# Kernel tuning notes

Hardware: AMD Instinct MI355X
Metric: run time of the kernel (lower is better)

The kernel has to match this reference:

```python
import jax, jax.numpy as jnp
import numpy as np

NEG = -1000000000.0
EPS = 1e-05

def setup_inputs() -> dict:
    key = jax.random.key(0)
    k1, k2, k3, k4, k5 = jax.random.split(key, 5)
    B, L, E, Q = 64, 2048, 512, 256
    encoded_vecs = jax.random.normal(k1, (B, L, E), dtype=jnp.float32)
    query = jax.random.normal(k2, (B, Q), dtype=jnp.float32)
    length = jax.random.randint(k3, (B,), 1, L + 1, dtype=jnp.int32)
    # Xavier-normal-ish params
    W1 = jax.random.normal(k4, (E + Q, E), dtype=jnp.float32) * jnp.sqrt(2.0 / (E + Q + E))
    b1 = jnp.zeros((E,), dtype=jnp.float32)
    v = jax.random.normal(k5, (E,), dtype=jnp.float32) * jnp.sqrt(2.0 / (E + 1))
    return {"encoded_vecs": encoded_vecs, "query": query, "length": length,
            "W1": W1, "b1": b1, "v": v}

def reference(encoded_vecs, query, length, W1, b1, v):
    B, L, E = encoded_vecs.shape
    # broadcast 2D query over the length dim (repeat in torch code)
    q = jnp.broadcast_to(query[:, None, :], (B, L, query.shape[-1]))
    h = jnp.concatenate([encoded_vecs, q], axis=2)            # [B, L, E+Q]
    u = jnp.tanh(jnp.einsum('blc,ce->ble', h, W1) + b1)       # [B, L, E]
    logits = jnp.einsum('ble,e->bl', u, v)                    # [B, L]
    # masked softmax (faithful to masked_softmax in source)
    mask = (jnp.arange(L)[None, :] < length[:, None])         # [B, L] bool
    masked_logits = jnp.where(mask, logits, NEG)
    max_logits = jnp.max(masked_logits, axis=1, keepdims=True)
    exps = jnp.exp(masked_logits - max_logits) * mask.astype(logits.dtype)
    attention = exps / (jnp.sum(exps, axis=1, keepdims=True) + EPS)  # [B, L]
    context = jnp.einsum('bl,ble->be', attention, encoded_vecs)      # [B, E]
    return (context, attention)
```

## Files before the change

### kernel.cpp

```cpp
#include <hip/hip_runtime.h>

typedef __attribute__((ext_vector_type(4))) float float4v;
typedef __attribute__((ext_vector_type(2))) float float2v;
typedef __attribute__((ext_vector_type(8))) short short8;
typedef __attribute__((ext_vector_type(4))) float f32x4;

#define NEGV (-1000000000.0f)

#define MTOT (64 * 2048)

__device__ __forceinline__ unsigned short f2bf(float f) {
    unsigned int u = __float_as_uint(f);
    u += 0x7fffu + ((u >> 16) & 1u);
    return (unsigned short)(u >> 16);
}

__device__ __forceinline__ void gload_lds16(const void* g, void* l) {
    __builtin_amdgcn_global_load_lds(
        (__attribute__((address_space(1))) unsigned int*)(unsigned long long)(g),
        (__attribute__((address_space(3))) unsigned int*)(unsigned int)(unsigned long long)(l),
        16, 0, 0);
}

__global__ __launch_bounds__(256)
void prep_wt_kernel(const float* __restrict__ W1, unsigned short* __restrict__ Wt) {
    __shared__ float t[32][33];
    int bx = blockIdx.x & 15;
    int by = blockIdx.x >> 4;
    int tx = threadIdx.x & 31;
    int ty = threadIdx.x >> 5;
    #pragma unroll
    for (int i = 0; i < 4; ++i)
        t[ty + 8 * i][tx] = W1[(bx * 32 + ty + 8 * i) * 512 + by * 32 + tx];
    __syncthreads();
    #pragma unroll
    for (int i = 0; i < 4; ++i)
        Wt[(by * 32 + ty + 8 * i) * 512 + bx * 32 + tx] = f2bf(t[tx][ty + 8 * i]);
}

__global__ void prep_qc_kernel(const float* __restrict__ query, const float* __restrict__ W1,
                               const float* __restrict__ b1, float* __restrict__ qc,
                               float* __restrict__ ctxraw, float* __restrict__ S) {
    int b = blockIdx.x;
    int e = threadIdx.x;
    ctxraw[b * 512 + e] = 0.f;
    ctxraw[b * 512 + 256 + e] = 0.f;
    if (e == 0) S[b] = 0.f;
    float acc0 = b1[e];
    float acc1 = b1[e + 256];
    const float* w = W1 + 512 * 512;
    #pragma unroll 8
    for (int q = 0; q < 256; ++q) {
        float qv = query[b * 256 + q];
        acc0 += qv * w[q * 512 + e];
        acc1 += qv * w[q * 512 + e + 256];
    }
    qc[b * 512 + e] = acc0;
    qc[b * 512 + e + 256] = acc1;
}

__global__ __launch_bounds__(1024)
void gemm_fused_kernel(const float* __restrict__ A,
                       const unsigned short* __restrict__ Wt,
                       const float* __restrict__ qc,
                       const float* __restrict__ v,
                       const int* __restrict__ length,
                       float* __restrict__ att,
                       float* __restrict__ ctxraw,
                       float* __restrict__ S)
{
    int bm = blockIdx.x;
    int b = bm >> 4;
    int len = length[b];
    int l0 = (bm & 15) * 128;
    if (l0 >= len) return;

    __shared__ char smem[73728];
    unsigned short* As = (unsigned short*)smem;
    unsigned short* Bs = (unsigned short*)(smem + 8192);
    float (*lred)[8] = (float(*)[8])(smem + 8192);
    float* wbuf = (float*)(smem + 8192 + 4096);

    int tid = threadIdx.x;
    int lane = tid & 63;
    int w = tid >> 6;
    int wm = w >> 3, wn = w & 7;
    long row0 = (long)bm * 128;

    int ar_r = tid >> 3;
    int ar_e = tid & 7;
    const char* gAr = (const char*)A + (row0 + ar_r) * 2048 + ar_e * 16;
    int awr = ar_r * 64 + ((ar_e * 8) ^ (((ar_r >> 1) & 3) << 4));

    int offw = w * 2048 + lane * 16;
    const char* gB0;
    const char* gB1;
    {
        int o = offw;
        int r = o >> 6;
        gB0 = (const char*)Wt + r * 1024 + ((o & 63) ^ (((r >> 1) & 3) << 4));
        o = offw + 1024;
        r = o >> 6;
        gB1 = (const char*)Wt + r * 1024 + ((o & 63) ^ (((r >> 1) & 3) << 4));
    }

    int aoff[4], boff[4];
    int kb = 16 * (lane >> 4);
    #pragma unroll
    for (int mi = 0; mi < 4; ++mi) {
        int ar = wm * 64 + (lane & 15) + mi * 16;
        aoff[mi] = ar * 64 + (kb ^ (((ar >> 1) & 3) << 4));
    }
    #pragma unroll
    for (int ni = 0; ni < 4; ++ni) {
        int br = wn * 64 + (lane & 15) + ni * 16;
        boff[ni] = br * 64 + (kb ^ (((br >> 1) & 3) << 4));
    }

    f32x4 acc[4][4] = {};
    float4v P;

#define GISSUE(t, sI) do {                                                   \
    P = *(const float4v*)(gAr + (t) * 128);                                  \
    char* lb_ = (char*)Bs + (sI) * 32768 + offw;                             \
    gload_lds16(gB0 + (t) * 64, lb_);                                        \
    gload_lds16(gB1 + (t) * 64, lb_ + 1024);                                 \
} while (0)

#define CVTW() do {                                                          \
    union { unsigned int u[2]; unsigned long long ll; } pk_;                 \
    pk_.u[0] = (unsigned int)f2bf(P[0]) | ((unsigned int)f2bf(P[1]) << 16);  \
    pk_.u[1] = (unsigned int)f2bf(P[2]) | ((unsigned int)f2bf(P[3]) << 16);  \
    *(unsigned long long*)((char*)As + awr) = pk_.ll;                        \
} while (0)

#define KCOMP(sC) do {                                                       \
    const char* as_ = (const char*)As;                                       \
    const char* bs_ = (const char*)Bs + (sC) * 32768;                        \
    short8 af_[4];                                                           \
    _Pragma("unroll")                                                        \
    for (int mi = 0; mi < 4; ++mi) af_[mi] = *(const short8*)(as_ + aoff[mi]); \
    _Pragma("unroll")                                                        \
    for (int ni = 0; ni < 4; ++ni) {                                         \
        short8 bf_ = *(const short8*)(bs_ + boff[ni]);                       \
        _Pragma("unroll")                                                    \
        for (int mi = 0; mi < 4; ++mi)                                       \
            acc[mi][ni] = __builtin_amdgcn_mfma_f32_16x16x32_bf16(af_[mi], bf_, acc[mi][ni], 0, 0, 0); \
    }                                                                        \
} while (0)

#define KITER(t) do {                                                        \
    GISSUE((t) + 1, ((t) + 1) & 1);                                          \
    KCOMP((t) & 1);                                                          \
    asm volatile("" ::: "memory");                                           \
    __builtin_amdgcn_s_barrier();                                            \
    asm volatile("s_waitcnt vmcnt(2)" ::: "memory");                         \
    CVTW();                                                                  \
    asm volatile("s_waitcnt vmcnt(0) lgkmcnt(0)" ::: "memory");              \
    __builtin_amdgcn_s_barrier();                                            \
    asm volatile("" ::: "memory");                                           \
} while (0)

    GISSUE(0, 0);
    asm volatile("s_waitcnt vmcnt(2)" ::: "memory");
    CVTW();
    asm volatile("s_waitcnt vmcnt(0) lgkmcnt(0)" ::: "memory");
    __builtin_amdgcn_s_barrier();
    asm volatile("" ::: "memory");

    KITER(0);  KITER(1);  KITER(2);  KITER(3);
    KITER(4);  KITER(5);  KITER(6);  KITER(7);
    KITER(8);  KITER(9);  KITER(10); KITER(11);
    KITER(12); KITER(13); KITER(14);
    KCOMP(1);

    const float* qcb = qc + b * 512;
    float vcol[4], qcol[4];
    #pragma unroll
    for (int ni = 0; ni < 4; ++ni) {
        int c = wn * 64 + ni * 16 + (lane & 15);
        vcol[ni] = v[c];
        qcol[ni] = qcb[c];
    }
    #pragma unroll
    for (int mi = 0; mi < 4; ++mi) {
        #pragma unroll
        for (int j2 = 0; j2 < 4; ++j2) {
            float s = 0.f;
            #pragma unroll
            for (int ni = 0; ni < 4; ++ni) {
                float xx = acc[mi][ni][j2] + qcol[ni];
                float e2 = __expf(2.0f * xx);
                float tt = 1.0f - 2.0f * __builtin_amdgcn_rcpf(e2 + 1.0f);
                s += tt * vcol[ni];
            }
            s += __shfl_xor(s, 1);
            s += __shfl_xor(s, 2);
            s += __shfl_xor(s, 4);
            s += __shfl_xor(s, 8);
            if ((lane & 15) == 0)
                lred[wm * 64 + mi * 16 + 4 * (lane >> 4) + j2][wn] = s;
        }
    }
    __syncthreads();

    if (tid < 128) {
        float lg = 0.f;
        #pragma unroll
        for (int q = 0; q < 8; ++q) lg += lred[tid][q];
        float wf = (l0 + tid < len) ? __expf(lg) : 0.f;
        att[row0 + tid] = wf;
        wbuf[tid] = wf;
        float s = wf;
        #pragma unroll
        for (int m = 32; m; m >>= 1) s += __shfl_xor(s, m);
        if ((tid & 63) == 0) atomicAdd(&S[b], s);
    }
    __syncthreads();

    {
        int e = tid & 511;
        int lh = tid >> 9;
        const float* encb = A + (row0 + lh * 64) * 512 + e;
        const float* wb = &wbuf[lh * 64];
        float c = 0.f;
        #pragma unroll 4
        for (int l = 0; l < 64; ++l)
            c += wb[l] * encb[l * 512];
        atomicAdd(&ctxraw[b * 512 + e], c);
    }
}

__global__ void norm_kernel(const float* __restrict__ S, const int* __restrict__ length,
                            const float* __restrict__ ctxraw,
                            float* __restrict__ att, float* __restrict__ ctx) {
    int b = blockIdx.x;
    int tid = threadIdx.x;
    float inv = 1.0f / S[b];
    ctx[b * 512 + tid] = ctxraw[b * 512 + tid] * inv;
    ctx[b * 512 + 256 + tid] = ctxraw[b * 512 + 256 + tid] * inv;
    int len = length[b];
    float* ab = att + b * 2048;
    #pragma unroll
    for (int i = 0; i < 8; ++i) {
        int l = tid + i * 256;
        float wv = ab[l];
        ab[l] = (l < len) ? wv * inv : 0.f;
    }
}

extern "C" void kernel_launch(void* const* d_in, const int* in_sizes, int n_in,
                              void* d_out, int out_size, void* d_ws, size_t ws_size,
                              hipStream_t stream) {
    const float* enc    = (const float*)d_in[0];
    const float* query  = (const float*)d_in[1];
    const int*   length = (const int*)d_in[2];
    const float* W1     = (const float*)d_in[3];
    const float* b1     = (const float*)d_in[4];
    const float* v      = (const float*)d_in[5];

    float* out = (float*)d_out;
    float* ctx = out;
    float* att = out + 64 * 512;

    char* ws = (char*)d_ws;
    float* qc          = (float*)ws;
    unsigned short* Wt = (unsigned short*)(ws + 64 * 512 * 4);
    float* ctxraw      = (float*)(ws + 64 * 512 * 4 + 512 * 1024);
    float* S           = (float*)(ws + 64 * 512 * 4 + 512 * 1024 + 64 * 512 * 4);

    prep_wt_kernel<<<256, 256, 0, stream>>>(W1, Wt);
    prep_qc_kernel<<<64, 256, 0, stream>>>(query, W1, b1, qc, ctxraw, S);

    gemm_fused_kernel<<<1024, 1024, 0, stream>>>(enc, Wt, qc, v, length, att, ctxraw, S);

    norm_kernel<<<64, 256, 0, stream>>>(S, length, ctxraw, att, ctx);
}
```

Before: 139.3 us.

## Halve GEMM row tile to 64 with 512-thread blocks and deeper A prefetch

The fused GEMM block now covers 64 rows instead of 128 and uses 8 waves, each owning a 64-column slice over all 64 rows. There are twice as many blocks, so length masking can skip work at a finer granularity and tail imbalance shrinks. The A tile is now prefetched two K-steps ahead through alternating registers, which needs new waitcnt values. In exchange, each 32KB B tile loaded per K-step is reused across half as many rows, doubling W traffic per row.

```diff
diff --git a/kernel.cpp b/kernel.cpp
--- a/kernel.cpp
+++ b/kernel.cpp
@@ -59,7 +59,7 @@
     qc[b * 512 + e + 256] = acc1;
 }
 
-__global__ __launch_bounds__(1024)
+__global__ __launch_bounds__(512)
 void gemm_fused_kernel(const float* __restrict__ A,
                        const unsigned short* __restrict__ Wt,
                        const float* __restrict__ qc,
@@ -70,67 +70,67 @@
                        float* __restrict__ S)
 {
     int bm = blockIdx.x;
-    int b = bm >> 4;
+    int b = bm >> 5;
     int len = length[b];
-    int l0 = (bm & 15) * 128;
+    int l0 = (bm & 31) * 64;
     if (l0 >= len) return;
 
-    __shared__ char smem[73728];
+    __shared__ char smem[69632];
     unsigned short* As = (unsigned short*)smem;
-    unsigned short* Bs = (unsigned short*)(smem + 8192);
-    float (*lred)[8] = (float(*)[8])(smem + 8192);
-    float* wbuf = (float*)(smem + 8192 + 4096);
+    unsigned short* Bs = (unsigned short*)(smem + 4096);
+    float (*lred)[8] = (float(*)[8])(smem + 4096);
+    float* wbuf = (float*)(smem + 4096 + 2048);
 
     int tid = threadIdx.x;
     int lane = tid & 63;
     int w = tid >> 6;
-    int wm = w >> 3, wn = w & 7;
-    long row0 = (long)bm * 128;
+    long row0 = (long)bm * 64;
 
     int ar_r = tid >> 3;
     int ar_e = tid & 7;
     const char* gAr = (const char*)A + (row0 + ar_r) * 2048 + ar_e * 16;
     int awr = ar_r * 64 + ((ar_e * 8) ^ (((ar_r >> 1) & 3) << 4));
 
-    int offw = w * 2048 + lane * 16;
-    const char* gB0;
-    const char* gB1;
-    {
-        int o = offw;
+    const char* gBsrc[4];
+    int boffs[4];
+    #pragma unroll
+    for (int i = 0; i < 4; ++i) {
+        int o = w * 4096 + i * 1024 + lane * 16;
         int r = o >> 6;
-        gB0 = (const char*)Wt + r * 1024 + ((o & 63) ^ (((r >> 1) & 3) << 4));
-        o = offw + 1024;
-        r = o >> 6;
-        gB1 = (const char*)Wt + r * 1024 + ((o & 63) ^ (((r >> 1) & 3) << 4));
+        boffs[i] = o;
+        gBsrc[i] = (const char*)Wt + r * 1024 + ((o & 63) ^ (((r >> 1) & 3) << 4));
     }
 
     int aoff[4], boff[4];
     int kb = 16 * (lane >> 4);
     #pragma unroll
     for (int mi = 0; mi < 4; ++mi) {
-        int ar = wm * 64 + (lane & 15) + mi * 16;
+        int ar = mi * 16 + (lane & 15);
         aoff[mi] = ar * 64 + (kb ^ (((ar >> 1) & 3) << 4));
     }
     #pragma unroll
     for (int ni = 0; ni < 4; ++ni) {
-        int br = wn * 64 + (lane & 15) + ni * 16;
+        int br = w * 64 + ni * 16 + (lane & 15);
         boff[ni] = br * 64 + (kb ^ (((br >> 1) & 3) << 4));
     }
 
     f32x4 acc[4][4] = {};
-    float4v P;
-
-#define GISSUE(t, sI) do {                                                   \
-    P = *(const float4v*)(gAr + (t) * 128);                                  \
-    char* lb_ = (char*)Bs + (sI) * 32768 + offw;                             \
-    gload_lds16(gB0 + (t) * 64, lb_);                                        \
-    gload_lds16(gB1 + (t) * 64, lb_ + 1024);                                 \
-} while (0)
-
-#define CVTW() do {                                                          \
+    float4v Pa, Pb;
+
+#define ALOAD(t_, P_) do { P_ = *(const float4v*)(gAr + (t_) * 128); } while (0)
+
+#define BISSUE(t_, sI) do {                                                  \
+    char* lb_ = (char*)Bs + (sI) * 32768;                                    \
+    gload_lds16(gBsrc[0] + (t_) * 64, lb_ + boffs[0]);                       \
+    gload_lds16(gBsrc[1] + (t_) * 64, lb_ + boffs[1]);                       \
+    gload_lds16(gBsrc[2] + (t_) * 64, lb_ + boffs[2]);                       \
+    gload_lds16(gBsrc[3] + (t_) * 64, lb_ + boffs[3]);                       \
+} while (0)
+
+#define CVTW(P_) do {                                                        \
     union { unsigned int u[2]; unsigned long long ll; } pk_;                 \
-    pk_.u[0] = (unsigned int)f2bf(P[0]) | ((unsigned int)f2bf(P[1]) << 16);  \
-    pk_.u[1] = (unsigned int)f2bf(P[2]) | ((unsigned int)f2bf(P[3]) << 16);  \
+    pk_.u[0] = (unsigned int)f2bf(P_[0]) | ((unsigned int)f2bf(P_[1]) << 16); \
+    pk_.u[1] = (unsigned int)f2bf(P_[2]) | ((unsigned int)f2bf(P_[3]) << 16); \
     *(unsigned long long*)((char*)As + awr) = pk_.ll;                        \
 } while (0)
 
@@ -149,36 +149,50 @@
     }                                                                        \
 } while (0)
 
-#define KITER(t) do {                                                        \
-    GISSUE((t) + 1, ((t) + 1) & 1);                                          \
+#define KITER(t, PI, PC, AISS, VM1, VM2) do {                                \
+    if (AISS) ALOAD((t) + 2, PI);                                            \
+    BISSUE((t) + 1, ((t) + 1) & 1);                                          \
     KCOMP((t) & 1);                                                          \
     asm volatile("" ::: "memory");                                           \
     __builtin_amdgcn_s_barrier();                                            \
-    asm volatile("s_waitcnt vmcnt(2)" ::: "memory");                         \
-    CVTW();                                                                  \
-    asm volatile("s_waitcnt vmcnt(0) lgkmcnt(0)" ::: "memory");              \
+    asm volatile("s_waitcnt vmcnt(" #VM1 ")" ::: "memory");                  \
+    CVTW(PC);                                                                \
+    asm volatile("s_waitcnt vmcnt(" #VM2 ") lgkmcnt(0)" ::: "memory");       \
     __builtin_amdgcn_s_barrier();                                            \
     asm volatile("" ::: "memory");                                           \
 } while (0)
 
-    GISSUE(0, 0);
-    asm volatile("s_waitcnt vmcnt(2)" ::: "memory");
-    CVTW();
-    asm volatile("s_waitcnt vmcnt(0) lgkmcnt(0)" ::: "memory");
+    ALOAD(0, Pa);
+    ALOAD(1, Pb);
+    BISSUE(0, 0);
+    asm volatile("s_waitcnt vmcnt(5)" ::: "memory");
+    CVTW(Pa);
+    asm volatile("s_waitcnt vmcnt(1) lgkmcnt(0)" ::: "memory");
     __builtin_amdgcn_s_barrier();
     asm volatile("" ::: "memory");
 
-    KITER(0);  KITER(1);  KITER(2);  KITER(3);
-    KITER(4);  KITER(5);  KITER(6);  KITER(7);
-    KITER(8);  KITER(9);  KITER(10); KITER(11);
-    KITER(12); KITER(13); KITER(14);
+    KITER(0,  Pa, Pb, 1, 5, 1);
+    KITER(1,  Pb, Pa, 1, 5, 1);
+    KITER(2,  Pa, Pb, 1, 5, 1);
+    KITER(3,  Pb, Pa, 1, 5, 1);
+    KITER(4,  Pa, Pb, 1, 5, 1);
+    KITER(5,  Pb, Pa, 1, 5, 1);
+    KITER(6,  Pa, Pb, 1, 5, 1);
+    KITER(7,  Pb, Pa, 1, 5, 1);
+    KITER(8,  Pa, Pb, 1, 5, 1);
+    KITER(9,  Pb, Pa, 1, 5, 1);
+    KITER(10, Pa, Pb, 1, 5, 1);
+    KITER(11, Pb, Pa, 1, 5, 1);
+    KITER(12, Pa, Pb, 1, 5, 1);
+    KITER(13, Pb, Pa, 1, 5, 1);
+    KITER(14, Pa, Pb, 0, 4, 0);
     KCOMP(1);
 
     const float* qcb = qc + b * 512;
     float vcol[4], qcol[4];
     #pragma unroll
     for (int ni = 0; ni < 4; ++ni) {
-        int c = wn * 64 + ni * 16 + (lane & 15);
+        int c = w * 64 + ni * 16 + (lane & 15);
         vcol[ni] = v[c];
         qcol[ni] = qcb[c];
     }
@@ -199,12 +213,12 @@
             s += __shfl_xor(s, 4);
             s += __shfl_xor(s, 8);
             if ((lane & 15) == 0)
-                lred[wm * 64 + mi * 16 + 4 * (lane >> 4) + j2][wn] = s;
+                lred[mi * 16 + 4 * (lane >> 4) + j2][w] = s;
         }
     }
     __syncthreads();
 
-    if (tid < 128) {
+    if (tid < 64) {
         float lg = 0.f;
         #pragma unroll
         for (int q = 0; q < 8; ++q) lg += lred[tid][q];
@@ -214,20 +228,17 @@
         float s = wf;
         #pragma unroll
         for (int m = 32; m; m >>= 1) s += __shfl_xor(s, m);
-        if ((tid & 63) == 0) atomicAdd(&S[b], s);
+        if (tid == 0) atomicAdd(&S[b], s);
     }
     __syncthreads();
 
     {
-        int e = tid & 511;
-        int lh = tid >> 9;
-        const float* encb = A + (row0 + lh * 64) * 512 + e;
-        const float* wb = &wbuf[lh * 64];
+        const float* encb = A + row0 * 512 + tid;
         float c = 0.f;
         #pragma unroll 4
         for (int l = 0; l < 64; ++l)
-            c += wb[l] * encb[l * 512];
-        atomicAdd(&ctxraw[b * 512 + e], c);
+            c += wbuf[l] * encb[l * 512];
+        atomicAdd(&ctxraw[b * 512 + tid], c);
     }
 }
 
@@ -272,7 +283,7 @@
     prep_wt_kernel<<<256, 256, 0, stream>>>(W1, Wt);
     prep_qc_kernel<<<64, 256, 0, stream>>>(query, W1, b1, qc, ctxraw, S);
 
-    gemm_fused_kernel<<<1024, 1024, 0, stream>>>(enc, Wt, qc, v, length, att, ctxraw, S);
+    gemm_fused_kernel<<<2048, 512, 0, stream>>>(enc, Wt, qc, v, length, att, ctxraw, S);
 
     norm_kernel<<<64, 256, 0, stream>>>(S, length, ctxraw, att, ctx);
 }
```

Measured after the change: 139.8 us. No clear change (+0.4%).

## Deepen GEMM pipeline to four B stages and split query projection across blocks

Applied to the files above, without the earlier changes.

The fused GEMM kernel now keeps four LDS stages for the bf16 weight tiles and two register buffers for the activation tiles. Loads are issued two to three K-steps ahead, and the waitcnt thresholds are relaxed so memory latency can overlap more MFMA work. Shared memory grows to 139 KB per block, which limits the kernel to one 1024-thread block per CU. The query projection is split into four K-chunks per batch that combine through atomicAdd, and a new init kernel seeds qc with the bias and zeroes the accumulators, at the cost of one extra launch.

```diff
diff --git a/kernel.cpp b/kernel.cpp
--- a/kernel.cpp
+++ b/kernel.cpp
@@ -20,6 +20,18 @@
         (__attribute__((address_space(1))) unsigned int*)(unsigned long long)(g),
         (__attribute__((address_space(3))) unsigned int*)(unsigned int)(unsigned long long)(l),
         16, 0, 0);
+}
+
+__global__ __launch_bounds__(256)
+void init_kernel(const float* __restrict__ b1, float* __restrict__ qc,
+                 float* __restrict__ ctxraw, float* __restrict__ S) {
+    int i = blockIdx.x * 256 + threadIdx.x;
+    if (i < 32768) {
+        qc[i] = b1[i & 511];
+    } else {
+        ctxraw[i - 32768] = 0.f;
+    }
+    if (i < 64) S[i] = 0.f;
 }
 
 __global__ __launch_bounds__(256)
@@ -38,25 +50,24 @@
         Wt[(by * 32 + ty + 8 * i) * 512 + bx * 32 + tx] = f2bf(t[tx][ty + 8 * i]);
 }
 
-__global__ void prep_qc_kernel(const float* __restrict__ query, const float* __restrict__ W1,
-                               const float* __restrict__ b1, float* __restrict__ qc,
-                               float* __restrict__ ctxraw, float* __restrict__ S) {
-    int b = blockIdx.x;
+__global__ __launch_bounds__(256)
+void prep_qc_kernel(const float* __restrict__ query, const float* __restrict__ W1,
+                    float* __restrict__ qc) {
+    int blk = blockIdx.x;
+    int b = blk >> 2;
+    int q0 = (blk & 3) * 64;
     int e = threadIdx.x;
-    ctxraw[b * 512 + e] = 0.f;
-    ctxraw[b * 512 + 256 + e] = 0.f;
-    if (e == 0) S[b] = 0.f;
-    float acc0 = b1[e];
-    float acc1 = b1[e + 256];
-    const float* w = W1 + 512 * 512;
+    float acc0 = 0.f, acc1 = 0.f;
+    const float* w = W1 + (512 + q0) * 512;
+    const float* qv = query + b * 256 + q0;
     #pragma unroll 8
-    for (int q = 0; q < 256; ++q) {
-        float qv = query[b * 256 + q];
-        acc0 += qv * w[q * 512 + e];
-        acc1 += qv * w[q * 512 + e + 256];
-    }
-    qc[b * 512 + e] = acc0;
-    qc[b * 512 + e + 256] = acc1;
+    for (int q = 0; q < 64; ++q) {
+        float x = qv[q];
+        acc0 += x * w[q * 512 + e];
+        acc1 += x * w[q * 512 + e + 256];
+    }
+    atomicAdd(&qc[b * 512 + e], acc0);
+    atomicAdd(&qc[b * 512 + e + 256], acc1);
 }
 
 __global__ __launch_bounds__(1024)
@@ -75,7 +86,7 @@
     int l0 = (bm & 15) * 128;
     if (l0 >= len) return;
 
-    __shared__ char smem[73728];
+    __shared__ char smem[139264];
     unsigned short* As = (unsigned short*)smem;
     unsigned short* Bs = (unsigned short*)(smem + 8192);
     float (*lred)[8] = (float(*)[8])(smem + 8192);
@@ -118,19 +129,20 @@
     }
 
     f32x4 acc[4][4] = {};
-    float4v P;
-
-#define GISSUE(t, sI) do {                                                   \
-    P = *(const float4v*)(gAr + (t) * 128);                                  \
+    float4v Pa, Pb;
+
+#define ALOAD(t_, P_) do { P_ = *(const float4v*)(gAr + (t_) * 128); } while (0)
+
+#define BISSUE(t_, sI) do {                                                  \
     char* lb_ = (char*)Bs + (sI) * 32768 + offw;                             \
-    gload_lds16(gB0 + (t) * 64, lb_);                                        \
-    gload_lds16(gB1 + (t) * 64, lb_ + 1024);                                 \
+    gload_lds16(gB0 + (t_) * 64, lb_);                                       \
+    gload_lds16(gB1 + (t_) * 64, lb_ + 1024);                                \
 } while (0)
 
-#define CVTW() do {                                                          \
+#define CVTW(P_) do {                                                        \
     union { unsigned int u[2]; unsigned long long ll; } pk_;                 \
-    pk_.u[0] = (unsigned int)f2bf(P[0]) | ((unsigned int)f2bf(P[1]) << 16);  \
-    pk_.u[1] = (unsigned int)f2bf(P[2]) | ((unsigned int)f2bf(P[3]) << 16);  \
+    pk_.u[0] = (unsigned int)f2bf(P_[0]) | ((unsigned int)f2bf(P_[1]) << 16); \
+    pk_.u[1] = (unsigned int)f2bf(P_[2]) | ((unsigned int)f2bf(P_[3]) << 16); \
     *(unsigned long long*)((char*)As + awr) = pk_.ll;                        \
 } while (0)
 
@@ -149,30 +161,46 @@
     }                                                                        \
 } while (0)
 
-#define KITER(t) do {                                                        \
-    GISSUE((t) + 1, ((t) + 1) & 1);                                          \
-    KCOMP((t) & 1);                                                          \
+#define KITER(t, PI, PC, AISS, BISS, VM) do {                                \
+    if (AISS) ALOAD((t) + 2, PI);                                            \
+    if (BISS) BISSUE((t) + 3, ((t) + 3) & 3);                                \
+    KCOMP((t) & 3);                                                          \
     asm volatile("" ::: "memory");                                           \
     __builtin_amdgcn_s_barrier();                                            \
-    asm volatile("s_waitcnt vmcnt(2)" ::: "memory");                         \
-    CVTW();                                                                  \
-    asm volatile("s_waitcnt vmcnt(0) lgkmcnt(0)" ::: "memory");              \
+    asm volatile("s_waitcnt vmcnt(" #VM ")" ::: "memory");                   \
+    CVTW(PC);                                                                \
+    asm volatile("s_waitcnt lgkmcnt(0)" ::: "memory");                       \
     __builtin_amdgcn_s_barrier();                                            \
     asm volatile("" ::: "memory");                                           \
 } while (0)
 
-    GISSUE(0, 0);
-    asm volatile("s_waitcnt vmcnt(2)" ::: "memory");
-    CVTW();
-    asm volatile("s_waitcnt vmcnt(0) lgkmcnt(0)" ::: "memory");
+    ALOAD(0, Pa);
+    ALOAD(1, Pb);
+    BISSUE(0, 0);
+    BISSUE(1, 1);
+    BISSUE(2, 2);
+    asm volatile("s_waitcnt vmcnt(4)" ::: "memory");
+    CVTW(Pa);
+    asm volatile("s_waitcnt lgkmcnt(0)" ::: "memory");
     __builtin_amdgcn_s_barrier();
     asm volatile("" ::: "memory");
 
-    KITER(0);  KITER(1);  KITER(2);  KITER(3);
-    KITER(4);  KITER(5);  KITER(6);  KITER(7);
-    KITER(8);  KITER(9);  KITER(10); KITER(11);
-    KITER(12); KITER(13); KITER(14);
-    KCOMP(1);
+    KITER(0,  Pa, Pb, 1, 1, 5);
+    KITER(1,  Pb, Pa, 1, 1, 5);
+    KITER(2,  Pa, Pb, 1, 1, 5);
+    KITER(3,  Pb, Pa, 1, 1, 5);
+    KITER(4,  Pa, Pb, 1, 1, 5);
+    KITER(5,  Pb, Pa, 1, 1, 5);
+    KITER(6,  Pa, Pb, 1, 1, 5);
+    KITER(7,  Pb, Pa, 1, 1, 5);
+    KITER(8,  Pa, Pb, 1, 1, 5);
+    KITER(9,  Pb, Pa, 1, 1, 5);
+    KITER(10, Pa, Pb, 1, 1, 5);
+    KITER(11, Pb, Pa, 1, 1, 5);
+    KITER(12, Pa, Pb, 1, 1, 5);
+    KITER(13, Pb, Pa, 1, 0, 3);
+    KITER(14, Pa, Pb, 0, 0, 0);
+    KCOMP(3);
 
     const float* qcb = qc + b * 512;
     float vcol[4], qcol[4];
@@ -269,8 +297,9 @@
     float* ctxraw      = (float*)(ws + 64 * 512 * 4 + 512 * 1024);
     float* S           = (float*)(ws + 64 * 512 * 4 + 512 * 1024 + 64 * 512 * 4);
 
+    init_kernel<<<256, 256, 0, stream>>>(b1, qc, ctxraw, S);
     prep_wt_kernel<<<256, 256, 0, stream>>>(W1, Wt);
-    prep_qc_kernel<<<64, 256, 0, stream>>>(query, W1, b1, qc, ctxraw, S);
+    prep_qc_kernel<<<256, 256, 0, stream>>>(query, W1, qc);
 
     gemm_fused_kernel<<<1024, 1024, 0, stream>>>(enc, Wt, qc, v, length, att, ctxraw, S);
 
```

After: 134.8 us. 1.03x faster.
